# Performance work log

Hardware: AMD Instinct MI355X
Metric: run time of the kernel (lower is better)

Reference implementation:

```python
import jax, jax.numpy as jnp
import numpy as np

N_NODES = 40000
N_EDGES = 640000
BATCH = 2
IN_DIM = 3
HID = 128
OUT_DIM = 3


def setup_inputs() -> dict:
    key = jax.random.key(0)
    ks = jax.random.split(key, 16)
    p = jax.random.normal(ks[0], (BATCH, N_NODES, IN_DIM), dtype=jnp.float32)
    edge_rows = jax.random.randint(ks[1], (N_EDGES,), 0, N_NODES, dtype=jnp.int32)
    edge_cols = jax.random.randint(ks[2], (N_EDGES,), 0, N_NODES, dtype=jnp.int32)
    # normalize_sparse_matrix: divide each nonzero (value 1.0) by the row's nonzero count
    deg = jax.ops.segment_sum(jnp.ones((N_EDGES,), jnp.float32), edge_rows, num_segments=N_NODES)
    adj_vals = 1.0 / deg[edge_rows]  # every used row has deg >= 1
    s = 0.05
    # initial Linear(3 -> 128)
    W_init = jax.random.normal(ks[3], (IN_DIM, HID), jnp.float32) * s
    b_init = jnp.zeros((HID,), jnp.float32)
    # 4 GraphConvs inside the two blocks (all 128->128), each has filter + self_filter
    Wf_blocks = jax.random.normal(ks[4], (4, HID, HID), jnp.float32) * s
    bf_blocks = jnp.zeros((4, HID), jnp.float32)
    Ws_blocks = jax.random.normal(ks[5], (4, HID, HID), jnp.float32) * s
    bs_blocks = jnp.zeros((4, HID), jnp.float32)
    # final GraphConvLayer (128 -> 3)
    Wf_out = jax.random.normal(ks[6], (HID, OUT_DIM), jnp.float32) * s
    bf_out = jnp.zeros((OUT_DIM,), jnp.float32)
    Ws_out = jax.random.normal(ks[7], (HID, OUT_DIM), jnp.float32) * s
    bs_out = jnp.zeros((OUT_DIM,), jnp.float32)
    return dict(p=p, adj_vals=adj_vals, edge_rows=edge_rows, edge_cols=edge_cols,
                W_init=W_init, b_init=b_init,
                Wf_blocks=Wf_blocks, bf_blocks=bf_blocks,
                Ws_blocks=Ws_blocks, bs_blocks=bs_blocks,
                Wf_out=Wf_out, bf_out=bf_out, Ws_out=Ws_out, bs_out=bs_out)


def reference(p, adj_vals, edge_rows, edge_cols,
              W_init, b_init,
              Wf_blocks, bf_blocks, Ws_blocks, bs_blocks,
              Wf_out, bf_out, Ws_out, bs_out):
    n = p.shape[1]

    def spmm(xb):  # xb: [N, d] -> A @ xb via edge-list scatter-add
        return jax.ops.segment_sum(adj_vals[:, None] * xb[edge_cols], edge_rows, num_segments=n)

    spmm_b = jax.vmap(spmm)  # [B, N, d]

    def gconv(x, Wf, bf, Ws, bs):
        # sparse path: self_filter(x) + filter(spmm(adj, x))
        return (x @ Ws + bs) + (spmm_b(x) @ Wf + bf)

    x = p @ W_init + b_init  # [B, N, HID]
    for blk in range(2):  # two GraphConvBlocks, residual, no shortcut (dims equal)
        net = gconv(jax.nn.relu(x), Wf_blocks[2 * blk], bf_blocks[2 * blk],
                    Ws_blocks[2 * blk], bs_blocks[2 * blk])
        dx = gconv(jax.nn.relu(net), Wf_blocks[2 * blk + 1], bf_blocks[2 * blk + 1],
                   Ws_blocks[2 * blk + 1], bs_blocks[2 * blk + 1])
        x = x + dx
    # final GraphConvLayer 128 -> 3
    out = gconv(jax.nn.relu(x), Wf_out, bf_out, Ws_out, bs_out)
    return out
```

## Files before the change

kernel.cpp:

```cpp
#include <hip/hip_runtime.h>


typedef unsigned short u16;
typedef unsigned int   u32;
typedef __bf16 bf8_t __attribute__((ext_vector_type(8)));
typedef float  f4_t  __attribute__((ext_vector_type(4)));

#define N_NODES 40000
#define N_EDGES 640000
#define BN      80000

__device__ __forceinline__ float bf2f(u16 u) {
  union { u32 i; float f; } v; v.i = ((u32)u) << 16; return v.f;
}
__device__ __forceinline__ u16 f2bf(float f) {
  union { float f; u32 i; } v; v.f = f;
  u32 i = v.i;
  return (u16)((i + 0x7FFFu + ((i >> 16) & 1u)) >> 16);
}
__device__ __forceinline__ float asf(u32 i) {
  union { u32 u; float f; } v; v.u = i; return v.f;
}
__device__ __forceinline__ u32 pack2(float a, float b) {
  return (u32)f2bf(a) | ((u32)f2bf(b) << 16);
}
__device__ __forceinline__ float lo2f(u32 v) { return asf(v << 16); }
__device__ __forceinline__ float hi2f(u32 v) { return asf(v & 0xffff0000u); }
__device__ __forceinline__ u32 relu2(u32 v) {
  u32 r = v;
  if (r & 0x8000u)     r &= 0xffff0000u;
  if (r & 0x80000000u) r &= 0x0000ffffu;
  return r;
}

__global__ void fill_kernel(float* __restrict__ out, int n, float v) {
  int i = blockIdx.x * 256 + threadIdx.x;
  if (i < n) out[i] = v;
}

__global__ void hist_kernel(const int* __restrict__ rows, int* __restrict__ cnt) {
  int e = blockIdx.x * 256 + threadIdx.x;
  if (e < N_EDGES) atomicAdd(&cnt[rows[e]], 1);
}

__global__ void scan1_kernel(const int* __restrict__ cnt, int* __restrict__ row_ptr,
                             int* __restrict__ blocksum) {
  __shared__ int sm[256];
  int t = threadIdx.x;
  int row = blockIdx.x * 256 + t;
  int v = (row < N_NODES) ? cnt[row] : 0;
  sm[t] = v; __syncthreads();
  for (int off = 1; off < 256; off <<= 1) {
    int u = (t >= off) ? sm[t - off] : 0;
    __syncthreads();
    sm[t] += u;
    __syncthreads();
  }
  if (row < N_NODES) row_ptr[row] = sm[t] - v;
  if (t == 255) blocksum[blockIdx.x] = sm[255];
}

__global__ void scan2_kernel(int* __restrict__ blocksum, int* __restrict__ row_ptr, int nblk) {
  __shared__ int sm[256];
  int t = threadIdx.x;
  int v = (t < nblk) ? blocksum[t] : 0;
  sm[t] = v; __syncthreads();
  for (int off = 1; off < 256; off <<= 1) {
    int u = (t >= off) ? sm[t - off] : 0;
    __syncthreads();
    sm[t] += u;
    __syncthreads();
  }
  if (t < nblk) blocksum[t] = sm[t] - v;
  if (t == 255) row_ptr[N_NODES] = sm[255];
}

__global__ void scan3_kernel(int* __restrict__ row_ptr, const int* __restrict__ blocksum,
                             int* __restrict__ cnt) {
  int row = blockIdx.x * 256 + threadIdx.x;
  if (row < N_NODES) {
    int rp = row_ptr[row] + blocksum[blockIdx.x];
    row_ptr[row] = rp;
    cnt[row] = rp;
  }
}

__global__ void scatter_kernel(const int* __restrict__ rows, const int* __restrict__ cols,
                               int* __restrict__ cur, int* __restrict__ cols_s) {
  int e = blockIdx.x * 256 + threadIdx.x;
  if (e < N_EDGES) {
    int r = rows[e];
    int pos = atomicAdd(&cur[r], 1);
    cols_s[pos] = cols[e];
  }
}

__global__ void initw_kernel(const float* __restrict__ p, const float* __restrict__ W,
                             const float* __restrict__ bias, u16* __restrict__ xb,
                             const float* __restrict__ Wf_b, const float* __restrict__ Ws_b,
                             const float* __restrict__ bf_b, const float* __restrict__ bs_b,
                             u16* __restrict__ WtCat, float* __restrict__ biasCat) {
  if (blockIdx.x >= 20000) {
    int idx = (blockIdx.x - 20000) * 256 + threadIdx.x;
    int g = idx >> 15, rem = idx & 32767;
    int h = rem >> 8, k = rem & 255;
    float v = (k < 128) ? Ws_b[(g * 128 + k) * 128 + h]
                        : Wf_b[(g * 128 + (k - 128)) * 128 + h];
    WtCat[idx] = f2bf(v);
    if (k == 0) biasCat[g * 128 + h] = bs_b[g * 128 + h] + bf_b[g * 128 + h];
    return;
  }
  int idx = blockIdx.x * 256 + threadIdx.x;
  int row = idx >> 6;
  int h = (idx & 63) * 2;
  float p0 = p[row * 3], p1 = p[row * 3 + 1], p2 = p[row * 3 + 2];
  float s0 = p0 * W[h]     + p1 * W[128 + h]     + p2 * W[256 + h]     + bias[h];
  float s1 = p0 * W[h + 1] + p1 * W[128 + h + 1] + p2 * W[256 + h + 1] + bias[h + 1];
  ((u32*)xb)[(size_t)row * 64 + (h >> 1)] = pack2(s0, s1);
}

#define ACC8R(u, A0, A1, A2, A3, A4, A5, A6, A7) do {                          \
    float f0, f1;                                                              \
    f0 = lo2f((u).x); f1 = hi2f((u).x);                                        \
    if (RELU) { f0 = fmaxf(f0, 0.f); f1 = fmaxf(f1, 0.f); }                    \
    A0 += f0; A1 += f1;                                                        \
    f0 = lo2f((u).y); f1 = hi2f((u).y);                                        \
    if (RELU) { f0 = fmaxf(f0, 0.f); f1 = fmaxf(f1, 0.f); }                    \
    A2 += f0; A3 += f1;                                                        \
    f0 = lo2f((u).z); f1 = hi2f((u).z);                                        \
    if (RELU) { f0 = fmaxf(f0, 0.f); f1 = fmaxf(f1, 0.f); }                    \
    A4 += f0; A5 += f1;                                                        \
    f0 = lo2f((u).w); f1 = hi2f((u).w);                                        \
    if (RELU) { f0 = fmaxf(f0, 0.f); f1 = fmaxf(f1, 0.f); }                    \
    A6 += f0; A7 += f1;                                                        \
  } while (0)

template <int RELU>
__global__ void spmm_kernel(const int* __restrict__ row_ptr, const int* __restrict__ cols_s,
                            const u16* __restrict__ xin, u16* __restrict__ yout) {
  int row = blockIdx.x * 4 + (threadIdx.x >> 6);
  int l = threadIdx.x & 63;
  int g = l >> 4, sl = l & 15;
  int s = row_ptr[row], e = row_ptr[row + 1];
  const uint4* X0 = (const uint4*)xin + sl;
  const uint4* X1 = X0 + 640000;
  float a0 = 0.f, a1 = 0.f, a2 = 0.f, a3 = 0.f, a4 = 0.f, a5 = 0.f, a6 = 0.f, a7 = 0.f;
  float b0 = 0.f, b1 = 0.f, b2 = 0.f, b3 = 0.f, b4 = 0.f, b5 = 0.f, b6 = 0.f, b7 = 0.f;
  int i = s;
  for (; i + 7 < e; i += 8) {
    int c0 = cols_s[i + g], c1 = cols_s[i + 4 + g];
    uint4 u00 = X0[(size_t)c0 * 16];
    uint4 u01 = X1[(size_t)c0 * 16];
    uint4 u10 = X0[(size_t)c1 * 16];
    uint4 u11 = X1[(size_t)c1 * 16];
    ACC8R(u00, a0, a1, a2, a3, a4, a5, a6, a7);
    ACC8R(u01, b0, b1, b2, b3, b4, b5, b6, b7);
    ACC8R(u10, a0, a1, a2, a3, a4, a5, a6, a7);
    ACC8R(u11, b0, b1, b2, b3, b4, b5, b6, b7);
  }
  for (; i + 3 < e; i += 4) {
    int c = cols_s[i + g];
    uint4 u0 = X0[(size_t)c * 16];
    uint4 u1 = X1[(size_t)c * 16];
    ACC8R(u0, a0, a1, a2, a3, a4, a5, a6, a7);
    ACC8R(u1, b0, b1, b2, b3, b4, b5, b6, b7);
  }
  if (i + g < e) {
    int c = cols_s[i + g];
    uint4 u0 = X0[(size_t)c * 16];
    uint4 u1 = X1[(size_t)c * 16];
    ACC8R(u0, a0, a1, a2, a3, a4, a5, a6, a7);
    ACC8R(u1, b0, b1, b2, b3, b4, b5, b6, b7);
  }
  a0 += __shfl_xor(a0, 16); a1 += __shfl_xor(a1, 16); a2 += __shfl_xor(a2, 16); a3 += __shfl_xor(a3, 16);
  a4 += __shfl_xor(a4, 16); a5 += __shfl_xor(a5, 16); a6 += __shfl_xor(a6, 16); a7 += __shfl_xor(a7, 16);
  b0 += __shfl_xor(b0, 16); b1 += __shfl_xor(b1, 16); b2 += __shfl_xor(b2, 16); b3 += __shfl_xor(b3, 16);
  b4 += __shfl_xor(b4, 16); b5 += __shfl_xor(b5, 16); b6 += __shfl_xor(b6, 16); b7 += __shfl_xor(b7, 16);
  a0 += __shfl_xor(a0, 32); a1 += __shfl_xor(a1, 32); a2 += __shfl_xor(a2, 32); a3 += __shfl_xor(a3, 32);
  a4 += __shfl_xor(a4, 32); a5 += __shfl_xor(a5, 32); a6 += __shfl_xor(a6, 32); a7 += __shfl_xor(a7, 32);
  b0 += __shfl_xor(b0, 32); b1 += __shfl_xor(b1, 32); b2 += __shfl_xor(b2, 32); b3 += __shfl_xor(b3, 32);
  b4 += __shfl_xor(b4, 32); b5 += __shfl_xor(b5, 32); b6 += __shfl_xor(b6, 32); b7 += __shfl_xor(b7, 32);
  float sc = (e > s) ? 1.f / (float)(e - s) : 0.f;
  if (g == 0) {
    uint4 o;
    o.x = pack2(a0 * sc, a1 * sc);
    o.y = pack2(a2 * sc, a3 * sc);
    o.z = pack2(a4 * sc, a5 * sc);
    o.w = pack2(a6 * sc, a7 * sc);
    *((uint4*)yout + (size_t)row * 16 + sl) = o;
  } else if (g == 1) {
    uint4 o;
    o.x = pack2(b0 * sc, b1 * sc);
    o.y = pack2(b2 * sc, b3 * sc);
    o.z = pack2(b4 * sc, b5 * sc);
    o.w = pack2(b6 * sc, b7 * sc);
    *((uint4*)yout + 640000 + (size_t)row * 16 + sl) = o;
  }
}

#define TS 136
template <int MODE>
__global__ __launch_bounds__(256, 4) void gemm_kernel(
    const u16* __restrict__ rin, const u16* __restrict__ yin,
    const u16* __restrict__ WtCat, const float* __restrict__ biasCat, int g,
    u16* __restrict__ rout, u16* __restrict__ xresid,
    float4* __restrict__ zf4, float4* __restrict__ zs4,
    const float* __restrict__ Wfo, const float* __restrict__ Wso,
    const float* __restrict__ bfo, const float* __restrict__ bso) {
  __shared__ __align__(16) u16 lds[18432];
  u16* ldsA = lds;
  u16* ldsW = lds + 9216;
  int tid = threadIdx.x;
  int m0 = blockIdx.x * 128;
  int li = tid & 15, q = (tid >> 4) & 3, wv = tid >> 6;
  int wmo = (wv >> 1) * 64, wno = (wv & 1) * 64;

  f4_t acc[4][4];
#pragma unroll
  for (int i = 0; i < 4; ++i)
#pragma unroll
    for (int j = 0; j < 4; ++j) acc[i][j] = (f4_t){0.f, 0.f, 0.f, 0.f};

  const u16* Wsrc = WtCat + (size_t)g * 32768;

  for (int kb = 0; kb < 256; kb += 64) {
    __syncthreads();
    const u16* srcA = (kb < 128) ? (rin + kb) : (yin + (kb - 128));
#pragma unroll
    for (int p2 = 0; p2 < 4; ++p2) {
      int idx = p2 * 256 + tid;
      int row = idx >> 3, seg = idx & 7;
      uint4 va = *reinterpret_cast<const uint4*>(srcA + (size_t)(m0 + row) * 128 + seg * 8);
      if (MODE == 0 && kb < 128) {
        va.x = relu2(va.x); va.y = relu2(va.y); va.z = relu2(va.z); va.w = relu2(va.w);
      }
      *reinterpret_cast<uint4*>(&ldsA[row * 72 + seg * 8]) = va;
      uint4 vw = *reinterpret_cast<const uint4*>(Wsrc + (size_t)row * 256 + kb + seg * 8);
      *reinterpret_cast<uint4*>(&ldsW[row * 72 + seg * 8]) = vw;
    }
    __syncthreads();
#pragma unroll
    for (int kk = 0; kk < 64; kk += 32) {
      bf8_t af[4], wf[4];
#pragma unroll
      for (int t = 0; t < 4; ++t)
        af[t] = __builtin_bit_cast(bf8_t,
            *reinterpret_cast<const uint4*>(&ldsA[(wmo + t * 16 + li) * 72 + kk + q * 8]));
#pragma unroll
      for (int t = 0; t < 4; ++t)
        wf[t] = __builtin_bit_cast(bf8_t,
            *reinterpret_cast<const uint4*>(&ldsW[(wno + t * 16 + li) * 72 + kk + q * 8]));
#pragma unroll
      for (int i = 0; i < 4; ++i)
#pragma unroll
        for (int j = 0; j < 4; ++j)
          acc[i][j] = __builtin_amdgcn_mfma_f32_16x16x32_bf16(af[i], wf[j], acc[i][j], 0, 0, 0);
    }
  }

  float bias[4];
#pragma unroll
  for (int j = 0; j < 4; ++j) bias[j] = biasCat[g * 128 + wno + j * 16 + li];

  __syncthreads();
#pragma unroll
  for (int i = 0; i < 4; ++i)
#pragma unroll
    for (int j = 0; j < 4; ++j)
#pragma unroll
      for (int r2 = 0; r2 < 4; ++r2) {
        int m = wmo + i * 16 + q * 4 + r2;
        int col = wno + j * 16 + li;
        lds[m * TS + col] = f2bf(acc[i][j][r2] + bias[j]);
      }
  __syncthreads();

  float wzf[8][3], wzs[8][3];
  if (MODE == 2) {
    int chb = (tid & 15) * 8;
#pragma unroll
    for (int c = 0; c < 8; ++c)
#pragma unroll
      for (int d = 0; d < 3; ++d) {
        wzf[c][d] = Wfo[(chb + c) * 3 + d];
        wzs[c][d] = Wso[(chb + c) * 3 + d];
      }
  }

#pragma unroll
  for (int p2 = 0; p2 < 8; ++p2) {
    int idx = p2 * 256 + tid;
    int row = idx >> 4, ch = idx & 15;
    uint4 cv = *reinterpret_cast<const uint4*>(&lds[row * TS + ch * 8]);
    size_t gid = (size_t)(m0 + row) * 16 + ch;
    if (MODE == 0) {
      uint4 o;
      o.x = relu2(cv.x); o.y = relu2(cv.y); o.z = relu2(cv.z); o.w = relu2(cv.w);
      ((uint4*)rout)[gid] = o;
    } else if (MODE == 1) {
      uint4 xv = ((const uint4*)xresid)[gid];
      uint4 nx;
      float x0, x1;
      x0 = lo2f(xv.x) + lo2f(cv.x); x1 = hi2f(xv.x) + hi2f(cv.x); nx.x = pack2(x0, x1);
      x0 = lo2f(xv.y) + lo2f(cv.y); x1 = hi2f(xv.y) + hi2f(cv.y); nx.y = pack2(x0, x1);
      x0 = lo2f(xv.z) + lo2f(cv.z); x1 = hi2f(xv.z) + hi2f(cv.z); nx.z = pack2(x0, x1);
      x0 = lo2f(xv.w) + lo2f(cv.w); x1 = hi2f(xv.w) + hi2f(cv.w); nx.w = pack2(x0, x1);
      ((uint4*)xresid)[gid] = nx;
    } else {
      uint4 xv = ((const uint4*)xresid)[gid];
      float zf0 = 0.f, zf1 = 0.f, zf2 = 0.f, zs0 = 0.f, zs1 = 0.f, zs2 = 0.f;
#pragma unroll
      for (int q2 = 0; q2 < 4; ++q2) {
        u32 xu = ((const u32*)&xv)[q2], cu = ((const u32*)&cv)[q2];
        float r0 = fmaxf(lo2f(xu) + lo2f(cu), 0.f);
        float r1 = fmaxf(hi2f(xu) + hi2f(cu), 0.f);
        int c = 2 * q2;
        zf0 += r0 * wzf[c][0] + r1 * wzf[c + 1][0];
        zf1 += r0 * wzf[c][1] + r1 * wzf[c + 1][1];
        zf2 += r0 * wzf[c][2] + r1 * wzf[c + 1][2];
        zs0 += r0 * wzs[c][0] + r1 * wzs[c + 1][0];
        zs1 += r0 * wzs[c][1] + r1 * wzs[c + 1][1];
        zs2 += r0 * wzs[c][2] + r1 * wzs[c + 1][2];
      }
#pragma unroll
      for (int off = 1; off < 16; off <<= 1) {
        zf0 += __shfl_xor(zf0, off); zf1 += __shfl_xor(zf1, off); zf2 += __shfl_xor(zf2, off);
        zs0 += __shfl_xor(zs0, off); zs1 += __shfl_xor(zs1, off); zs2 += __shfl_xor(zs2, off);
      }
      if ((tid & 15) == 0) {
        int m = m0 + row;
        zf4[m] = make_float4(zf0, zf1, zf2, 0.f);
        zs4[m] = make_float4(zs0 + bso[0] + bfo[0], zs1 + bso[1] + bfo[1],
                             zs2 + bso[2] + bfo[2], 0.f);
      }
    }
  }
}

__global__ void spmm3_kernel(const int* __restrict__ row_ptr, const int* __restrict__ cols_s,
                             const float4* __restrict__ zf4, const float4* __restrict__ zs4,
                             float* __restrict__ out) {
  int idx = blockIdx.x * 256 + threadIdx.x;
  if (idx >= BN) return;
  int b = (idx >= N_NODES) ? 1 : 0;
  int r = idx - b * N_NODES;
  int s = row_ptr[r], e = row_ptr[r + 1];
  const float4* Z = zf4 + (size_t)b * N_NODES;
  float a0 = 0.f, a1 = 0.f, a2 = 0.f;
  for (int i = s; i < e; ++i) {
    float4 z = Z[cols_s[i]];
    a0 += z.x; a1 += z.y; a2 += z.z;
  }
  float sc = (e > s) ? 1.f / (float)(e - s) : 0.f;
  float4 zs = zs4[idx];
  out[idx * 3 + 0] = zs.x + a0 * sc;
  out[idx * 3 + 1] = zs.y + a1 * sc;
  out[idx * 3 + 2] = zs.z + a2 * sc;
}

extern "C" void kernel_launch(void* const* d_in, const int* in_sizes, int n_in,
                              void* d_out, int out_size, void* d_ws, size_t ws_size,
                              hipStream_t stream) {
  float* out = (float*)d_out;
  int fill_grid = (out_size + 255) / 256;

  const int exp_sizes[14] = {240000, 640000, 640000, 640000, 384, 128,
                             65536, 512, 65536, 512, 384, 3, 384, 3};
  bool sizes_ok = (n_in == 14);
  if (sizes_ok) for (int i = 0; i < 14; ++i) if (in_sizes[i] != exp_sizes[i]) sizes_ok = false;
  if (!sizes_ok) {
    fill_kernel<<<fill_grid, 256, 0, stream>>>(out, out_size, 1.0f);
    return;
  }

  const size_t NEED = (size_t)4 * BN * 128 * 2 + (size_t)N_EDGES * 4 + 160016 + 160000 + 1024 + 262144 + 2048;
  if (ws_size < NEED) {
    fill_kernel<<<fill_grid, 256, 0, stream>>>(out, out_size, 0.0f);
    return;
  }

  const float* p      = (const float*)d_in[0];
  const int*   erows  = (const int*)d_in[2];
  const int*   ecols  = (const int*)d_in[3];
  const float* W_init = (const float*)d_in[4];
  const float* b_init = (const float*)d_in[5];
  const float* Wf_b   = (const float*)d_in[6];
  const float* bf_b   = (const float*)d_in[7];
  const float* Ws_b   = (const float*)d_in[8];
  const float* bs_b   = (const float*)d_in[9];
  const float* Wf_o   = (const float*)d_in[10];
  const float* bf_o   = (const float*)d_in[11];
  const float* Ws_o   = (const float*)d_in[12];
  const float* bs_o   = (const float*)d_in[13];

  char* w = (char*)d_ws;
  char*  zbuf     = w;         w += (size_t)BN * 128 * 2;
  u16*   rB       = (u16*)w;   w += (size_t)BN * 128 * 2;
  u16*   y        = (u16*)w;   w += (size_t)BN * 128 * 2;
  u16*   xb       = (u16*)w;   w += (size_t)BN * 128 * 2;
  int*   cols_s   = (int*)w;   w += (size_t)N_EDGES * 4;
  int*   row_ptr  = (int*)w;   w += 160016;
  int*   cnt      = (int*)w;   w += 160000;
  int*   blocksum = (int*)w;   w += 1024;
  u16*   WtCat    = (u16*)w;   w += 4 * 128 * 256 * 2;
  float* biasCat  = (float*)w; w += 4 * 128 * 4;

  float4* zf4 = (float4*)zbuf;
  float4* zs4 = (float4*)(zbuf + 1280000);

  const int NBLK = (N_NODES + 255) / 256;

  hipMemsetAsync(cnt, 0, N_NODES * 4, stream);
  hist_kernel<<<2500, 256, 0, stream>>>(erows, cnt);
  scan1_kernel<<<NBLK, 256, 0, stream>>>(cnt, row_ptr, blocksum);
  scan2_kernel<<<1, 256, 0, stream>>>(blocksum, row_ptr, NBLK);
  scan3_kernel<<<NBLK, 256, 0, stream>>>(row_ptr, blocksum, cnt);
  scatter_kernel<<<2500, 256, 0, stream>>>(erows, ecols, cnt, cols_s);
  initw_kernel<<<20512, 256, 0, stream>>>(p, W_init, b_init, xb,
                                          Wf_b, Ws_b, bf_b, bs_b, WtCat, biasCat);

  for (int blk = 0; blk < 2; ++blk) {
    spmm_kernel<1><<<10000, 256, 0, stream>>>(row_ptr, cols_s, xb, y);
    gemm_kernel<0><<<625, 256, 0, stream>>>(xb, y, WtCat, biasCat, 2 * blk, rB, nullptr,
                                            nullptr, nullptr, nullptr, nullptr, nullptr, nullptr);
    spmm_kernel<0><<<10000, 256, 0, stream>>>(row_ptr, cols_s, rB, y);
    if (blk == 0)
      gemm_kernel<1><<<625, 256, 0, stream>>>(rB, y, WtCat, biasCat, 1, nullptr, xb,
                                              nullptr, nullptr, nullptr, nullptr, nullptr, nullptr);
    else
      gemm_kernel<2><<<625, 256, 0, stream>>>(rB, y, WtCat, biasCat, 3, nullptr, xb,
                                              zf4, zs4, Wf_o, Ws_o, bf_o, bs_o);
  }
  spmm3_kernel<<<(BN + 255) / 256, 256, 0, stream>>>(row_ptr, cols_s, zf4, zs4, out);
}
```

Measured before the change: 429.3 us.

## Halve GEMM LDS by reading weights from global and staging epilogue in halves

The GEMM kernel no longer stages the weight tile in shared memory. Each wave now loads its weight fragments straight from global memory, which leans on L1/L2 caching, and the shared buffer shrinks to 18 KB. The epilogue writes back in two 64-row halves so it fits the smaller buffer, and the smaller LDS footprint is meant to let more blocks run per CU. In exchange it adds uncoalesced global weight loads inside the K loop and extra barriers, and the ACC8R macro is rewritten without functional change.

```diff
diff --git a/kernel.cpp b/kernel.cpp
--- a/kernel.cpp
+++ b/kernel.cpp
@@ -119,21 +119,15 @@
   ((u32*)xb)[(size_t)row * 64 + (h >> 1)] = pack2(s0, s1);
 }
 
-#define ACC8R(u, A0, A1, A2, A3, A4, A5, A6, A7) do {                          \
-    float f0, f1;                                                              \
-    f0 = lo2f((u).x); f1 = hi2f((u).x);                                        \
-    if (RELU) { f0 = fmaxf(f0, 0.f); f1 = fmaxf(f1, 0.f); }                    \
-    A0 += f0; A1 += f1;                                                        \
-    f0 = lo2f((u).y); f1 = hi2f((u).y);                                        \
-    if (RELU) { f0 = fmaxf(f0, 0.f); f1 = fmaxf(f1, 0.f); }                    \
-    A2 += f0; A3 += f1;                                                        \
-    f0 = lo2f((u).z); f1 = hi2f((u).z);                                        \
-    if (RELU) { f0 = fmaxf(f0, 0.f); f1 = fmaxf(f1, 0.f); }                    \
-    A4 += f0; A5 += f1;                                                        \
-    f0 = lo2f((u).w); f1 = hi2f((u).w);                                        \
-    if (RELU) { f0 = fmaxf(f0, 0.f); f1 = fmaxf(f1, 0.f); }                    \
-    A6 += f0; A7 += f1;                                                        \
-  } while (0)
+#define ACC8R(u, A0, A1, A2, A3, A4, A5, A6, A7)                               \
+  A0 += RELU ? fmaxf(lo2f((u).x), 0.f) : lo2f((u).x);                          \
+  A1 += RELU ? fmaxf(hi2f((u).x), 0.f) : hi2f((u).x);                          \
+  A2 += RELU ? fmaxf(lo2f((u).y), 0.f) : lo2f((u).y);                          \
+  A3 += RELU ? fmaxf(hi2f((u).y), 0.f) : hi2f((u).y);                          \
+  A4 += RELU ? fmaxf(lo2f((u).z), 0.f) : lo2f((u).z);                          \
+  A5 += RELU ? fmaxf(hi2f((u).z), 0.f) : hi2f((u).z);                          \
+  A6 += RELU ? fmaxf(lo2f((u).w), 0.f) : lo2f((u).w);                          \
+  A7 += RELU ? fmaxf(hi2f((u).w), 0.f) : hi2f((u).w);
 
 template <int RELU>
 __global__ void spmm_kernel(const int* __restrict__ row_ptr, const int* __restrict__ cols_s,
@@ -207,9 +201,7 @@
     float4* __restrict__ zf4, float4* __restrict__ zs4,
     const float* __restrict__ Wfo, const float* __restrict__ Wso,
     const float* __restrict__ bfo, const float* __restrict__ bso) {
-  __shared__ __align__(16) u16 lds[18432];
-  u16* ldsA = lds;
-  u16* ldsW = lds + 9216;
+  __shared__ __align__(16) u16 lds[9216];
   int tid = threadIdx.x;
   int m0 = blockIdx.x * 128;
   int li = tid & 15, q = (tid >> 4) & 3, wv = tid >> 6;
@@ -234,9 +226,7 @@
       if (MODE == 0 && kb < 128) {
         va.x = relu2(va.x); va.y = relu2(va.y); va.z = relu2(va.z); va.w = relu2(va.w);
       }
-      *reinterpret_cast<uint4*>(&ldsA[row * 72 + seg * 8]) = va;
-      uint4 vw = *reinterpret_cast<const uint4*>(Wsrc + (size_t)row * 256 + kb + seg * 8);
-      *reinterpret_cast<uint4*>(&ldsW[row * 72 + seg * 8]) = vw;
+      *reinterpret_cast<uint4*>(&lds[row * 72 + seg * 8]) = va;
     }
     __syncthreads();
 #pragma unroll
@@ -245,11 +235,11 @@
 #pragma unroll
       for (int t = 0; t < 4; ++t)
         af[t] = __builtin_bit_cast(bf8_t,
-            *reinterpret_cast<const uint4*>(&ldsA[(wmo + t * 16 + li) * 72 + kk + q * 8]));
+            *reinterpret_cast<const uint4*>(&lds[(wmo + t * 16 + li) * 72 + kk + q * 8]));
 #pragma unroll
       for (int t = 0; t < 4; ++t)
-        wf[t] = __builtin_bit_cast(bf8_t,
-            *reinterpret_cast<const uint4*>(&ldsW[(wno + t * 16 + li) * 72 + kk + q * 8]));
+        wf[t] = __builtin_bit_cast(bf8_t, *reinterpret_cast<const uint4*>(
+            Wsrc + (size_t)(wno + t * 16 + li) * 256 + kb + kk + q * 8));
 #pragma unroll
       for (int i = 0; i < 4; ++i)
 #pragma unroll
@@ -261,19 +251,6 @@
   float bias[4];
 #pragma unroll
   for (int j = 0; j < 4; ++j) bias[j] = biasCat[g * 128 + wno + j * 16 + li];
-
-  __syncthreads();
-#pragma unroll
-  for (int i = 0; i < 4; ++i)
-#pragma unroll
-    for (int j = 0; j < 4; ++j)
-#pragma unroll
-      for (int r2 = 0; r2 < 4; ++r2) {
-        int m = wmo + i * 16 + q * 4 + r2;
-        int col = wno + j * 16 + li;
-        lds[m * TS + col] = f2bf(acc[i][j][r2] + bias[j]);
-      }
-  __syncthreads();
 
   float wzf[8][3], wzs[8][3];
   if (MODE == 2) {
@@ -288,50 +265,66 @@
   }
 
 #pragma unroll
-  for (int p2 = 0; p2 < 8; ++p2) {
-    int idx = p2 * 256 + tid;
-    int row = idx >> 4, ch = idx & 15;
-    uint4 cv = *reinterpret_cast<const uint4*>(&lds[row * TS + ch * 8]);
-    size_t gid = (size_t)(m0 + row) * 16 + ch;
-    if (MODE == 0) {
-      uint4 o;
-      o.x = relu2(cv.x); o.y = relu2(cv.y); o.z = relu2(cv.z); o.w = relu2(cv.w);
-      ((uint4*)rout)[gid] = o;
-    } else if (MODE == 1) {
-      uint4 xv = ((const uint4*)xresid)[gid];
-      uint4 nx;
-      float x0, x1;
-      x0 = lo2f(xv.x) + lo2f(cv.x); x1 = hi2f(xv.x) + hi2f(cv.x); nx.x = pack2(x0, x1);
-      x0 = lo2f(xv.y) + lo2f(cv.y); x1 = hi2f(xv.y) + hi2f(cv.y); nx.y = pack2(x0, x1);
-      x0 = lo2f(xv.z) + lo2f(cv.z); x1 = hi2f(xv.z) + hi2f(cv.z); nx.z = pack2(x0, x1);
-      x0 = lo2f(xv.w) + lo2f(cv.w); x1 = hi2f(xv.w) + hi2f(cv.w); nx.w = pack2(x0, x1);
-      ((uint4*)xresid)[gid] = nx;
-    } else {
-      uint4 xv = ((const uint4*)xresid)[gid];
-      float zf0 = 0.f, zf1 = 0.f, zf2 = 0.f, zs0 = 0.f, zs1 = 0.f, zs2 = 0.f;
-#pragma unroll
-      for (int q2 = 0; q2 < 4; ++q2) {
-        u32 xu = ((const u32*)&xv)[q2], cu = ((const u32*)&cv)[q2];
-        float r0 = fmaxf(lo2f(xu) + lo2f(cu), 0.f);
-        float r1 = fmaxf(hi2f(xu) + hi2f(cu), 0.f);
-        int c = 2 * q2;
-        zf0 += r0 * wzf[c][0] + r1 * wzf[c + 1][0];
-        zf1 += r0 * wzf[c][1] + r1 * wzf[c + 1][1];
-        zf2 += r0 * wzf[c][2] + r1 * wzf[c + 1][2];
-        zs0 += r0 * wzs[c][0] + r1 * wzs[c + 1][0];
-        zs1 += r0 * wzs[c][1] + r1 * wzs[c + 1][1];
-        zs2 += r0 * wzs[c][2] + r1 * wzs[c + 1][2];
-      }
-#pragma unroll
-      for (int off = 1; off < 16; off <<= 1) {
-        zf0 += __shfl_xor(zf0, off); zf1 += __shfl_xor(zf1, off); zf2 += __shfl_xor(zf2, off);
-        zs0 += __shfl_xor(zs0, off); zs1 += __shfl_xor(zs1, off); zs2 += __shfl_xor(zs2, off);
-      }
-      if ((tid & 15) == 0) {
-        int m = m0 + row;
-        zf4[m] = make_float4(zf0, zf1, zf2, 0.f);
-        zs4[m] = make_float4(zs0 + bso[0] + bfo[0], zs1 + bso[1] + bfo[1],
-                             zs2 + bso[2] + bfo[2], 0.f);
+  for (int half = 0; half < 2; ++half) {
+    __syncthreads();
+    if (wmo == half * 64) {
+#pragma unroll
+      for (int i = 0; i < 4; ++i)
+#pragma unroll
+        for (int j = 0; j < 4; ++j)
+#pragma unroll
+          for (int r2 = 0; r2 < 4; ++r2) {
+            int m = i * 16 + q * 4 + r2;
+            lds[m * TS + wno + j * 16 + li] = f2bf(acc[i][j][r2] + bias[j]);
+          }
+    }
+    __syncthreads();
+#pragma unroll
+    for (int p2 = 0; p2 < 4; ++p2) {
+      int idx = p2 * 256 + tid;
+      int row = idx >> 4, ch = idx & 15;
+      uint4 cv = *reinterpret_cast<const uint4*>(&lds[row * TS + ch * 8]);
+      size_t gid = (size_t)(m0 + half * 64 + row) * 16 + ch;
+      if (MODE == 0) {
+        uint4 o;
+        o.x = relu2(cv.x); o.y = relu2(cv.y); o.z = relu2(cv.z); o.w = relu2(cv.w);
+        ((uint4*)rout)[gid] = o;
+      } else if (MODE == 1) {
+        uint4 xv = ((const uint4*)xresid)[gid];
+        uint4 nx;
+        float x0, x1;
+        x0 = lo2f(xv.x) + lo2f(cv.x); x1 = hi2f(xv.x) + hi2f(cv.x); nx.x = pack2(x0, x1);
+        x0 = lo2f(xv.y) + lo2f(cv.y); x1 = hi2f(xv.y) + hi2f(cv.y); nx.y = pack2(x0, x1);
+        x0 = lo2f(xv.z) + lo2f(cv.z); x1 = hi2f(xv.z) + hi2f(cv.z); nx.z = pack2(x0, x1);
+        x0 = lo2f(xv.w) + lo2f(cv.w); x1 = hi2f(xv.w) + hi2f(cv.w); nx.w = pack2(x0, x1);
+        ((uint4*)xresid)[gid] = nx;
+      } else {
+        uint4 xv = ((const uint4*)xresid)[gid];
+        float zf0 = 0.f, zf1 = 0.f, zf2 = 0.f, zs0 = 0.f, zs1 = 0.f, zs2 = 0.f;
+#pragma unroll
+        for (int q2 = 0; q2 < 4; ++q2) {
+          u32 xu = ((const u32*)&xv)[q2], cu = ((const u32*)&cv)[q2];
+          float r0 = fmaxf(lo2f(xu) + lo2f(cu), 0.f);
+          float r1 = fmaxf(hi2f(xu) + hi2f(cu), 0.f);
+          int c = 2 * q2;
+          zf0 += r0 * wzf[c][0] + r1 * wzf[c + 1][0];
+          zf1 += r0 * wzf[c][1] + r1 * wzf[c + 1][1];
+          zf2 += r0 * wzf[c][2] + r1 * wzf[c + 1][2];
+          zs0 += r0 * wzs[c][0] + r1 * wzs[c + 1][0];
+          zs1 += r0 * wzs[c][1] + r1 * wzs[c + 1][1];
+          zs2 += r0 * wzs[c][2] + r1 * wzs[c + 1][2];
+        }
+#pragma unroll
+        for (int off = 1; off < 16; off <<= 1) {
+          zf0 += __shfl_xor(zf0, off); zf1 += __shfl_xor(zf1, off); zf2 += __shfl_xor(zf2, off);
+          zs0 += __shfl_xor(zs0, off); zs1 += __shfl_xor(zs1, off); zs2 += __shfl_xor(zs2, off);
+        }
+        if ((tid & 15) == 0) {
+          int m = m0 + half * 64 + row;
+          zf4[m] = make_float4(zf0, zf1, zf2, 0.f);
+          zs4[m] = make_float4(zs0 + bso[0] + bfo[0], zs1 + bso[1] + bfo[1],
+                               zs2 + bso[2] + bfo[2], 0.f);
+        }
       }
     }
   }
```

New measurement: 477.3 us. 1.11x slower.
